# Performance work log

Measured on AMD Instinct MI355X. Metric: run time of the kernel, lower is better.

The kernel has to match this reference:

```python
import jax, jax.numpy as jnp
import numpy as np

N_TOKENS = 32768
DIM = 4096
N_EXPERTS = 64
TOPK = 2
UPDATE_BIAS_RATE = 0.001
ROUTE_SCALE = 1.0


def setup_inputs() -> dict:
    key = jax.random.key(0)
    k1, k2 = jax.random.split(key)
    x = jax.random.normal(k1, (N_TOKENS, DIM), dtype=jnp.float32)
    # gate projection weight, as in nn.Parameter(torch.empty(E, dim)) + kaiming init
    weight = jax.random.normal(k2, (N_EXPERTS, DIM), dtype=jnp.float32) * 0.02
    bias = jnp.zeros((N_EXPERTS,), dtype=jnp.float32)          # registered buffer
    target_dist = jnp.full((N_EXPERTS,), 1.0 / N_EXPERTS, dtype=jnp.float32)
    return {"x": x, "weight": weight, "bias": bias, "target_dist": target_dist}


def reference(x, weight, bias, target_dist):
    # scores = linear(nan_to_num(x), W) + bias, softmax in fp32
    xc = jnp.nan_to_num(x, nan=0.0)
    scores = (xc @ weight.T + bias).astype(jnp.float32)        # [N, E]
    probs = jax.nn.softmax(scores, axis=-1)                    # [N, E]
    # top-k: gathered values equal the top-k probabilities
    topv, indices = jax.lax.top_k(probs, TOPK)                 # [N, K], [N, K]
    weights = topv / jnp.sum(topv, axis=-1, keepdims=True)
    weights = weights * ROUTE_SCALE
    # load-balancing stats: bincount with float weights == segment_sum
    expert_weights_sum = jax.ops.segment_sum(
        weights.reshape(-1), indices.reshape(-1), num_segments=N_EXPERTS)
    total_weights = expert_weights_sum.sum()
    load_error = target_dist * total_weights - expert_weights_sum
    new_bias = bias + UPDATE_BIAS_RATE * (load_error / total_weights)
    return weights.astype(x.dtype), indices, new_bias
```

## Files before the change

### kernel.cpp

```cpp
#include <hip/hip_runtime.h>
#include <math.h>

#define N_TOKENS 32768
#define DIM      4096
#define NE       64
#define TM       64
#define BK       128
#define NBLK     (N_TOKENS / TM)
#define EPS_GAP  2e-3f
#define REFINE_BLOCKS 1024

#define WOFF 65664
#define WFRAG_ELEMS (512 * 512)

typedef __bf16 bf16x4 __attribute__((ext_vector_type(4)));
typedef __bf16 bf16x8 __attribute__((ext_vector_type(8)));
typedef float  f32x16 __attribute__((ext_vector_type(16)));

__global__ __launch_bounds__(256) void prep_w(
    const float* __restrict__ w, float* __restrict__ ws)
{
    __bf16* whi = (__bf16*)(ws + WOFF);
    __bf16* wlo = whi + WFRAG_ELEMS;
    const int tid  = blockIdx.x * 256 + threadIdx.x;
    const int f    = tid >> 6, lane = tid & 63;
    const int nt   = f & 1,    K16  = f >> 1;
    const int e    = nt * 32 + (lane & 31);
    const int k    = K16 * 16 + (lane >> 5) * 8;
    const float4 a = *(const float4*)(w + (size_t)e * DIM + k);
    const float4 b = *(const float4*)(w + (size_t)e * DIM + k + 4);
    const float v[8] = {a.x, a.y, a.z, a.w, b.x, b.y, b.z, b.w};
    bf16x8 h, l;
    #pragma unroll
    for (int i = 0; i < 8; ++i) {
        h[i] = (__bf16)v[i];
        l[i] = (__bf16)(v[i] - (float)h[i]);
    }
    *(bf16x8*)(whi + (size_t)tid * 8) = h;
    *(bf16x8*)(wlo + (size_t)tid * 8) = l;
}

__device__ __forceinline__ void cvt_split(const float4 v, bf16x4& h, bf16x4& l) {
    h[0] = (__bf16)v.x; l[0] = (__bf16)(v.x - (float)h[0]);
    h[1] = (__bf16)v.y; l[1] = (__bf16)(v.y - (float)h[1]);
    h[2] = (__bf16)v.z; l[2] = (__bf16)(v.z - (float)h[2]);
    h[3] = (__bf16)v.w; l[3] = (__bf16)(v.w - (float)h[3]);
}

__global__ __launch_bounds__(256) void gate_main(
    const float* __restrict__ x,
    const float* __restrict__ bias,
    float* __restrict__ out,
    float* __restrict__ ws)
{
    __shared__ __align__(16) unsigned char smem[32768];
    __shared__ float part[NE];
    __shared__ float sbias[NE];

    unsigned* wl_count = (unsigned*)(ws + 64);
    float*    partials = ws + 128;
    int*      wl       = (int*)(ws + 32896);
    const __bf16* whi  = (const __bf16*)(ws + WOFF);
    const __bf16* wlo  = whi + WFRAG_ELEMS;

    const int t    = threadIdx.x;
    const int lane = t & 63;
    const int wave = t >> 6;
    const int mt   = wave >> 1;
    const int nt   = wave & 1;
    const int tb   = blockIdx.x * TM;

    if (t < NE) { sbias[t] = bias[t]; part[t] = 0.f; }

    const int q     = t & 31;
    const int rbase = t >> 5;

    f32x16 acc0, acc1, acc2;
    #pragma unroll
    for (int i = 0; i < 16; ++i) { acc0[i] = 0.f; acc1[i] = 0.f; acc2[i] = 0.f; }

    float4 xv[8];
    #pragma unroll
    for (int j = 0; j < 8; ++j)
        xv[j] = *(const float4*)(x + (size_t)(tb + rbase + 8 * j) * DIM + q * 4);

    const int tok0  = mt * 32 + (lane & 31);
    const int klane = lane >> 5;
    const int abase = tok0 * 256;
    const int aswz  = (tok0 & 7) << 4;

    for (int kc = 0; kc < DIM; kc += BK) {
        #pragma unroll
        for (int j = 0; j < 8; ++j) {
            const int r = rbase + 8 * j;
            bf16x4 h, l;
            cvt_split(xv[j], h, l);
            const int off = r * 256 + ((q * 8) ^ ((r & 7) << 4));
            *(bf16x4*)(&smem[off])         = h;
            *(bf16x4*)(&smem[16384 + off]) = l;
        }
        __syncthreads();

        if (kc + BK < DIM) {
            #pragma unroll
            for (int j = 0; j < 8; ++j)
                xv[j] = *(const float4*)(x + (size_t)(tb + rbase + 8 * j) * DIM + kc + BK + q * 4);
        }

        const int K16c = kc >> 4;
        #pragma unroll
        for (int ks = 0; ks < 8; ++ks) {
            const int aoff = abase + ((ks * 32 + klane * 16) ^ aswz);
            const bf16x8 ah = *(const bf16x8*)(&smem[aoff]);
            const bf16x8 al = *(const bf16x8*)(&smem[16384 + aoff]);
            const size_t bidx = ((size_t)((K16c + ks) * 2 + nt) * 64 + lane) * 8;
            const bf16x8 bh = *(const bf16x8*)(whi + bidx);
            const bf16x8 bl = *(const bf16x8*)(wlo + bidx);
            acc0 = __builtin_amdgcn_mfma_f32_32x32x16_bf16(ah, bh, acc0, 0, 0, 0);
            acc1 = __builtin_amdgcn_mfma_f32_32x32x16_bf16(al, bh, acc1, 0, 0, 0);
            acc2 = __builtin_amdgcn_mfma_f32_32x32x16_bf16(ah, bl, acc2, 0, 0, 0);
        }
        __syncthreads();
    }

    float* sc = (float*)smem;
    const int e = nt * 32 + (lane & 31);
    #pragma unroll
    for (int r = 0; r < 16; ++r) {
        const int tok = mt * 32 + (r & 3) + 8 * (r >> 2) + 4 * (lane >> 5);
        sc[tok * 68 + e] = acc0[r] + acc1[r] + acc2[r];
    }
    __syncthreads();

    if (t < TM) {
        const int tok = t;
        float v1 = -3e38f, v2 = -3e38f, v3 = -3e38f;
        int   i1 = 0,      i2 = 0;
        #pragma unroll 8
        for (int ei = 0; ei < NE; ++ei) {
            const float s = sc[tok * 68 + ei] + sbias[ei];
            if (s > v1)      { v3 = v2; v2 = v1; i2 = i1; v1 = s; i1 = ei; }
            else if (s > v2) { v3 = v2; v2 = s;  i2 = ei; }
            else if (s > v3) { v3 = s; }
        }
        const bool risky = (v1 - v2 < EPS_GAP) || (v2 - v3 < EPS_GAP);
        if (risky) {
            const int pos = (int)atomicAdd(wl_count, 1u);
            wl[pos] = tb + tok;
        } else {
            const float ex = expf(v2 - v1);
            const float w1 = 1.f / (1.f + ex);
            const float w2 = ex * w1;
            const size_t g = (size_t)(tb + tok) * 2;
            *(float2*)(out + g)                        = make_float2(w1, w2);
            *(float2*)(out + (size_t)N_TOKENS * 2 + g) = make_float2((float)i1, (float)i2);
            atomicAdd(&part[i1], w1);
            atomicAdd(&part[i2], w2);
        }
    }
    __syncthreads();

    if (t < NE) partials[(size_t)blockIdx.x * NE + t] = part[t];
}

__global__ __launch_bounds__(256) void gate_refine(
    const float* __restrict__ x,
    const float* __restrict__ w,
    const float* __restrict__ bias,
    float* __restrict__ out,
    float* __restrict__ ws)
{
    float*          ews_ref  = ws;
    const unsigned* wl_count = (const unsigned*)(ws + 64);
    const int*      wl       = (const int*)(ws + 32896);

    const int t = threadIdx.x;
    const int e = t >> 2;
    const int q = t & 3;
    __shared__ double sc[NE];

    const unsigned count = *wl_count;
    for (unsigned it = blockIdx.x; it < count; it += gridDim.x) {
        const int tok = wl[it];
        const float* xr = x + (size_t)tok * DIM;
        const float* wr = w + (size_t)e * DIM;
        double s = 0.0;
        const int k0 = q * (DIM / 4), k1 = k0 + DIM / 4;
        for (int k = k0; k < k1; k += 4) {
            const float4 a = *(const float4*)(xr + k);
            const float4 b = *(const float4*)(wr + k);
            s += (double)a.x * (double)b.x;
            s += (double)a.y * (double)b.y;
            s += (double)a.z * (double)b.z;
            s += (double)a.w * (double)b.w;
        }
        s += __shfl_xor(s, 1);
        s += __shfl_xor(s, 2);
        if (q == 0) sc[e] = s + (double)bias[e];
        __syncthreads();

        if (t == 0) {
            double v1 = -1e300, v2 = -1e300;
            int i1 = 0, i2 = 0;
            for (int j = 0; j < NE; ++j) {
                const double sv = sc[j];
                if (sv > v1)      { v2 = v1; i2 = i1; v1 = sv; i1 = j; }
                else if (sv > v2) { v2 = sv; i2 = j; }
            }
            const double ex = exp(v2 - v1);
            const double w1 = 1.0 / (1.0 + ex);
            const double w2 = ex * w1;
            const size_t g = (size_t)tok * 2;
            *(float2*)(out + g)                        = make_float2((float)w1, (float)w2);
            *(float2*)(out + (size_t)N_TOKENS * 2 + g) = make_float2((float)i1, (float)i2);
            atomicAdd(&ews_ref[i1], (float)w1);
            atomicAdd(&ews_ref[i2], (float)w2);
        }
        __syncthreads();
    }
}

__global__ void gate_bias(
    const float* __restrict__ bias,
    const float* __restrict__ target,
    const float* __restrict__ ws,
    float* __restrict__ out)
{
    const int e = threadIdx.x;
    const float* partials = ws + 128;
    float v = ws[e];
    for (int b = 0; b < NBLK; ++b) v += partials[(size_t)b * NE + e];
    float total = v;
    #pragma unroll
    for (int off = 32; off > 0; off >>= 1)
        total += __shfl_xor(total, off);
    const float nb = bias[e] + 0.001f * ((target[e] * total - v) / total);
    out[(size_t)N_TOKENS * 4 + e] = nb;
}

extern "C" void kernel_launch(void* const* d_in, const int* in_sizes, int n_in,
                              void* d_out, int out_size, void* d_ws, size_t ws_size,
                              hipStream_t stream) {
    const float* x      = (const float*)d_in[0];
    const float* w      = (const float*)d_in[1];
    const float* bias   = (const float*)d_in[2];
    const float* target = (const float*)d_in[3];
    float* out = (float*)d_out;
    float* ws  = (float*)d_ws;

    hipMemsetAsync(ws, 0, 128 * sizeof(float), stream);
    prep_w     <<<128, 256, 0, stream>>>(w, ws);
    gate_main  <<<NBLK, 256, 0, stream>>>(x, bias, out, ws);
    gate_refine<<<REFINE_BLOCKS, 256, 0, stream>>>(x, w, bias, out, ws);
    gate_bias  <<<1, 64, 0, stream>>>(bias, target, ws, out);
}
```

Baseline: 287.3 us.

## Split GEMM K dimension across two blocks and move top-k into separate post kernel

Result: faster. 281.4 us (-2.0%).

```diff
diff --git a/kernel.cpp b/kernel.cpp
--- a/kernel.cpp
+++ b/kernel.cpp
@@ -6,11 +6,16 @@
 #define NE       64
 #define TM       64
 #define BK       128
-#define NBLK     (N_TOKENS / TM)
+#define KHALF    (DIM / 2)
+#define NBLK_MAIN (N_TOKENS / TM * 2)
+#define NBLK_POST (N_TOKENS / 256)
 #define EPS_GAP  2e-3f
 #define REFINE_BLOCKS 1024
 
-#define WOFF 65664
+#define WOFF     65664
+#define WL_OFF   16384
+#define PART_OFF 128
+#define PSC_OFF  524288
 #define WFRAG_ELEMS (512 * 512)
 
 typedef __bf16 bf16x4 __attribute__((ext_vector_type(4)));
@@ -47,49 +52,43 @@
     h[3] = (__bf16)v.w; l[3] = (__bf16)(v.w - (float)h[3]);
 }
 
-__global__ __launch_bounds__(256) void gate_main(
+__global__ __launch_bounds__(256, 4) void gate_main(
     const float* __restrict__ x,
-    const float* __restrict__ bias,
-    float* __restrict__ out,
     float* __restrict__ ws)
 {
     __shared__ __align__(16) unsigned char smem[32768];
-    __shared__ float part[NE];
-    __shared__ float sbias[NE];
-
-    unsigned* wl_count = (unsigned*)(ws + 64);
-    float*    partials = ws + 128;
-    int*      wl       = (int*)(ws + 32896);
-    const __bf16* whi  = (const __bf16*)(ws + WOFF);
-    const __bf16* wlo  = whi + WFRAG_ELEMS;
+
+    const __bf16* whi = (const __bf16*)(ws + WOFF);
+    const __bf16* wlo = whi + WFRAG_ELEMS;
+    float*        psc = ws + PSC_OFF;
 
     const int t    = threadIdx.x;
     const int lane = t & 63;
     const int wave = t >> 6;
     const int mt   = wave >> 1;
     const int nt   = wave & 1;
-    const int tb   = blockIdx.x * TM;
-
-    if (t < NE) { sbias[t] = bias[t]; part[t] = 0.f; }
+    const int kh   = blockIdx.x & 1;
+    const int tb   = (blockIdx.x >> 1) * TM;
+    const int kbeg = kh * KHALF;
 
     const int q     = t & 31;
     const int rbase = t >> 5;
 
-    f32x16 acc0, acc1, acc2;
-    #pragma unroll
-    for (int i = 0; i < 16; ++i) { acc0[i] = 0.f; acc1[i] = 0.f; acc2[i] = 0.f; }
+    f32x16 acc0, acc12;
+    #pragma unroll
+    for (int i = 0; i < 16; ++i) { acc0[i] = 0.f; acc12[i] = 0.f; }
 
     float4 xv[8];
     #pragma unroll
     for (int j = 0; j < 8; ++j)
-        xv[j] = *(const float4*)(x + (size_t)(tb + rbase + 8 * j) * DIM + q * 4);
+        xv[j] = *(const float4*)(x + (size_t)(tb + rbase + 8 * j) * DIM + kbeg + q * 4);
 
     const int tok0  = mt * 32 + (lane & 31);
     const int klane = lane >> 5;
     const int abase = tok0 * 256;
     const int aswz  = (tok0 & 7) << 4;
 
-    for (int kc = 0; kc < DIM; kc += BK) {
+    for (int kc = kbeg; kc < kbeg + KHALF; kc += BK) {
         #pragma unroll
         for (int j = 0; j < 8; ++j) {
             const int r = rbase + 8 * j;
@@ -101,7 +100,7 @@
         }
         __syncthreads();
 
-        if (kc + BK < DIM) {
+        if (kc + BK < kbeg + KHALF) {
             #pragma unroll
             for (int j = 0; j < 8; ++j)
                 xv[j] = *(const float4*)(x + (size_t)(tb + rbase + 8 * j) * DIM + kc + BK + q * 4);
@@ -116,50 +115,73 @@
             const size_t bidx = ((size_t)((K16c + ks) * 2 + nt) * 64 + lane) * 8;
             const bf16x8 bh = *(const bf16x8*)(whi + bidx);
             const bf16x8 bl = *(const bf16x8*)(wlo + bidx);
-            acc0 = __builtin_amdgcn_mfma_f32_32x32x16_bf16(ah, bh, acc0, 0, 0, 0);
-            acc1 = __builtin_amdgcn_mfma_f32_32x32x16_bf16(al, bh, acc1, 0, 0, 0);
-            acc2 = __builtin_amdgcn_mfma_f32_32x32x16_bf16(ah, bl, acc2, 0, 0, 0);
-        }
-        __syncthreads();
-    }
-
-    float* sc = (float*)smem;
+            acc0  = __builtin_amdgcn_mfma_f32_32x32x16_bf16(ah, bh, acc0,  0, 0, 0);
+            acc12 = __builtin_amdgcn_mfma_f32_32x32x16_bf16(al, bh, acc12, 0, 0, 0);
+            acc12 = __builtin_amdgcn_mfma_f32_32x32x16_bf16(ah, bl, acc12, 0, 0, 0);
+        }
+        __syncthreads();
+    }
+
     const int e = nt * 32 + (lane & 31);
+    float* base = psc + (size_t)kh * N_TOKENS * NE;
     #pragma unroll
     for (int r = 0; r < 16; ++r) {
         const int tok = mt * 32 + (r & 3) + 8 * (r >> 2) + 4 * (lane >> 5);
-        sc[tok * 68 + e] = acc0[r] + acc1[r] + acc2[r];
-    }
+        base[(size_t)(tb + tok) * NE + e] = acc0[r] + acc12[r];
+    }
+}
+
+__global__ __launch_bounds__(256) void gate_post(
+    const float* __restrict__ bias,
+    float* __restrict__ out,
+    float* __restrict__ ws)
+{
+    __shared__ float sbias[NE];
+    __shared__ float part[NE];
+    unsigned* wl_count = (unsigned*)(ws + 64);
+    float*    partials = ws + PART_OFF;
+    int*      wl       = (int*)(ws + WL_OFF);
+    const float* psc   = ws + PSC_OFF;
+
+    const int t = threadIdx.x;
+    if (t < NE) { sbias[t] = bias[t]; part[t] = 0.f; }
     __syncthreads();
 
-    if (t < TM) {
-        const int tok = t;
-        float v1 = -3e38f, v2 = -3e38f, v3 = -3e38f;
-        int   i1 = 0,      i2 = 0;
-        #pragma unroll 8
-        for (int ei = 0; ei < NE; ++ei) {
-            const float s = sc[tok * 68 + ei] + sbias[ei];
-            if (s > v1)      { v3 = v2; v2 = v1; i2 = i1; v1 = s; i1 = ei; }
-            else if (s > v2) { v3 = v2; v2 = s;  i2 = ei; }
-            else if (s > v3) { v3 = s; }
-        }
-        const bool risky = (v1 - v2 < EPS_GAP) || (v2 - v3 < EPS_GAP);
-        if (risky) {
-            const int pos = (int)atomicAdd(wl_count, 1u);
-            wl[pos] = tb + tok;
-        } else {
-            const float ex = expf(v2 - v1);
-            const float w1 = 1.f / (1.f + ex);
-            const float w2 = ex * w1;
-            const size_t g = (size_t)(tb + tok) * 2;
-            *(float2*)(out + g)                        = make_float2(w1, w2);
-            *(float2*)(out + (size_t)N_TOKENS * 2 + g) = make_float2((float)i1, (float)i2);
-            atomicAdd(&part[i1], w1);
-            atomicAdd(&part[i2], w2);
-        }
+    const int tok = blockIdx.x * 256 + t;
+    const float* p0 = psc + (size_t)tok * NE;
+    const float* p1 = psc + (size_t)N_TOKENS * NE + (size_t)tok * NE;
+
+    float v1 = -3e38f, v2 = -3e38f, v3 = -3e38f;
+    int   i1 = 0,      i2 = 0;
+    #pragma unroll
+    for (int g = 0; g < 16; ++g) {
+        const float4 a = *(const float4*)(p0 + g * 4);
+        const float4 b = *(const float4*)(p1 + g * 4);
+        float s[4] = {a.x + b.x, a.y + b.y, a.z + b.z, a.w + b.w};
+        #pragma unroll
+        for (int j = 0; j < 4; ++j) {
+            const float sv = s[j] + sbias[g * 4 + j];
+            const int   e  = g * 4 + j;
+            if (sv > v1)      { v3 = v2; v2 = v1; i2 = i1; v1 = sv; i1 = e; }
+            else if (sv > v2) { v3 = v2; v2 = sv; i2 = e; }
+            else if (sv > v3) { v3 = sv; }
+        }
+    }
+    const bool risky = (v1 - v2 < EPS_GAP) || (v2 - v3 < EPS_GAP);
+    if (risky) {
+        const int pos = (int)atomicAdd(wl_count, 1u);
+        wl[pos] = tok;
+    } else {
+        const float ex = expf(v2 - v1);
+        const float w1 = 1.f / (1.f + ex);
+        const float w2 = ex * w1;
+        const size_t g = (size_t)tok * 2;
+        *(float2*)(out + g)                        = make_float2(w1, w2);
+        *(float2*)(out + (size_t)N_TOKENS * 2 + g) = make_float2((float)i1, (float)i2);
+        atomicAdd(&part[i1], w1);
+        atomicAdd(&part[i2], w2);
     }
     __syncthreads();
-
     if (t < NE) partials[(size_t)blockIdx.x * NE + t] = part[t];
 }
 
@@ -172,7 +194,7 @@
 {
     float*          ews_ref  = ws;
     const unsigned* wl_count = (const unsigned*)(ws + 64);
-    const int*      wl       = (const int*)(ws + 32896);
+    const int*      wl       = (const int*)(ws + WL_OFF);
 
     const int t = threadIdx.x;
     const int e = t >> 2;
@@ -227,9 +249,9 @@
     float* __restrict__ out)
 {
     const int e = threadIdx.x;
-    const float* partials = ws + 128;
+    const float* partials = ws + PART_OFF;
     float v = ws[e];
-    for (int b = 0; b < NBLK; ++b) v += partials[(size_t)b * NE + e];
+    for (int b = 0; b < NBLK_POST; ++b) v += partials[(size_t)b * NE + e];
     float total = v;
     #pragma unroll
     for (int off = 32; off > 0; off >>= 1)
@@ -250,7 +272,8 @@
 
     hipMemsetAsync(ws, 0, 128 * sizeof(float), stream);
     prep_w     <<<128, 256, 0, stream>>>(w, ws);
-    gate_main  <<<NBLK, 256, 0, stream>>>(x, bias, out, ws);
+    gate_main  <<<NBLK_MAIN, 256, 0, stream>>>(x, ws);
+    gate_post  <<<NBLK_POST, 256, 0, stream>>>(bias, out, ws);
     gate_refine<<<REFINE_BLOCKS, 256, 0, stream>>>(x, w, bias, out, ws);
     gate_bias  <<<1, 64, 0, stream>>>(bias, target, ws, out);
 }
```
